# Performance work log

Hardware: AMD Instinct MI355X
Metric: run time of the kernel (lower is better)

Reference implementation:

```python
import jax, jax.numpy as jnp
import numpy as np

B, N, DIM, HEADS = 2, 2048, 1024, 16
HD = DIM // HEADS
STEPS, DT = 10, 0.1
PI = np.float32(np.pi)
SCALE = HD ** -0.5


def l2norm(x, eps=1e-12):
    # torch F.normalize: x / max(||x||_2, eps), works for complex via |x|^2
    n = jnp.sqrt(jnp.sum(jnp.abs(x) ** 2, axis=-1, keepdims=True))
    return x / jnp.maximum(n, eps)


def setup_inputs() -> dict:
    key = jax.random.key(0)
    ks = jax.random.split(key, 6)
    x = jax.random.normal(ks[0], (B, N, DIM), dtype=jnp.float32)
    Wqkv = jax.random.normal(ks[1], (DIM, 3 * DIM), dtype=jnp.float32) * (DIM ** -0.5)
    bqkv = jnp.zeros((3 * DIM,), dtype=jnp.float32)
    Wp1 = jax.random.normal(ks[2], (HD, 2 * HD), dtype=jnp.float32) * (HD ** -0.5)
    bp1 = jnp.zeros((2 * HD,), dtype=jnp.float32)
    Wp2 = jax.random.normal(ks[3], (2 * HD, HD), dtype=jnp.float32) * ((2 * HD) ** -0.5)
    bp2 = jnp.zeros((HD,), dtype=jnp.float32)
    Wf = jax.random.normal(ks[4], (HD, HD), dtype=jnp.float32) * (HD ** -0.5)
    return {"x": x, "Wqkv": Wqkv, "bqkv": bqkv, "Wp1": Wp1, "bp1": bp1,
            "Wp2": Wp2, "bp2": bp2, "Wf": Wf}


def _forward(x, Wqkv, bqkv, Wp1, bp1, Wp2, bp2, Wf):
    # qkv projection + normalize over last dim of the concatenated qkv
    qkv = l2norm(x @ Wqkv + bqkv)                      # [B,N,3*DIM]
    q, k, v = jnp.split(qkv, 3, axis=-1)

    def split_heads(t):
        return t.reshape(B, N, HEADS, HD).transpose(0, 2, 1, 3)  # [B,H,N,D]

    q, k, v = split_heads(q), split_heads(k), split_heads(v)

    def prepare_quantum_state(t):
        phase = jnp.tanh(t @ Wp1 + bp1) @ Wp2 + bp2    # phase-net MLP
        amplitude = l2norm(t)
        phase = jnp.tanh(phase) * PI
        return amplitude * jnp.exp(1j * phase)         # complex64 state

    q, k, v = prepare_quantum_state(q), prepare_quantum_state(k), prepare_quantum_state(v)

    def geometric_flow(z):
        # 10-step Euler integration of linear geometric velocity field
        for _ in range(STEPS):
            z = z + DT * (z @ Wf.astype(z.dtype))
        return l2norm(z)

    q = geometric_flow(q)
    k = geometric_flow(k)

    # parallel_transport(k, q): complex elementwise square -> complex dist
    diff = k - q
    dist = jnp.sqrt(jnp.sum(diff * diff, axis=-1, keepdims=True))
    tf = 1.0 / (1.0 + jnp.exp(10.0 * dist))            # sigmoid(-10*dist)
    k_t = l2norm(k * tf + q * (1.0 - tf))

    dots = (jnp.einsum('bhnd,bhmd->bhnm', q, k_t) * SCALE).real
    attn = jax.nn.softmax(dots, axis=-1)               # dropout in eval mode
    v = jnp.abs(v)                                     # magnitude of values
    out = jnp.einsum('bhnm,bhmd->bhnd', attn, v)
    return out.transpose(0, 2, 1, 3).reshape(B, N, DIM)


def reference(x, Wqkv, bqkv, Wp1, bp1, Wp2, bp2, Wf):
    return _forward(x, Wqkv, bqkv, Wp1, bp1, Wp2, bp2, Wf)
```

## Files before the change

kernel.cpp:

```cpp
#include <hip/hip_runtime.h>
#include <math.h>

#define B_    2
#define N_    2048
#define DIM_  1024
#define H_    16
#define HD_   64
#define TDIM  3072
#define ROWS  4096
#define PI_F  3.14159265358979323846f
#define SCALE_F 0.125f

typedef short short8 __attribute__((ext_vector_type(8)));
typedef float f32x4 __attribute__((ext_vector_type(4)));
typedef float f32x16 __attribute__((ext_vector_type(16)));
typedef unsigned u32x4 __attribute__((ext_vector_type(4)));
typedef unsigned short ushort_t;

__device__ __forceinline__ float wave_sum(float v) {
#pragma unroll
  for (int off = 32; off > 0; off >>= 1) v += __shfl_xor(v, off, 64);
  return v;
}

__device__ __forceinline__ unsigned short f2bf(float x) {
  return (unsigned short)((__float_as_uint(x) + 0x8000u) >> 16);
}
__device__ __forceinline__ float bf2f(unsigned short h) {
  return __uint_as_float(((unsigned)h) << 16);
}
__device__ __forceinline__ float inv_norm(float s) {
  return __builtin_amdgcn_rsqf(fmaxf(s, 1e-24f));
}
__device__ __forceinline__ float fast_tanh(float x) {
  return 1.0f - 2.0f / (__expf(2.0f * x) + 1.0f);
}

__device__ __forceinline__ void gl_lds16(const void* g, void* l) {
  __builtin_amdgcn_global_load_lds(
      (const __attribute__((address_space(1))) unsigned int*)g,
      (__attribute__((address_space(3))) unsigned int*)l, 16, 0, 0);
}

__global__ __launch_bounds__(256) void zero_sumsq(float* __restrict__ s) {
  const int i = threadIdx.x;
#pragma unroll
  for (int j = 0; j < 16; ++j) s[j * 256 + i] = 0.0f;
}

__global__ __launch_bounds__(256) void compute_M(const float* __restrict__ Wf,
                                                 ushort_t* __restrict__ Ms) {
  __shared__ float P[4096], Q[4096], R[4096];
  const int tid = threadIdx.x;
  for (int i = tid; i < 4096; i += 256)
    P[i] = 0.1f * Wf[i] + (((i >> 6) == (i & 63)) ? 1.0f : 0.0f);
  __syncthreads();

#define MATMUL64(X, Y, Z) \
  for (int i = tid; i < 4096; i += 256) { \
    const int r_ = i >> 6, c_ = i & 63; \
    float s0 = 0.f, s1 = 0.f, s2 = 0.f, s3 = 0.f; \
    _Pragma("unroll") \
    for (int e = 0; e < 64; e += 4) { \
      s0 = fmaf(X[r_ * 64 + e],     Y[e * 64 + c_], s0); \
      s1 = fmaf(X[r_ * 64 + e + 1], Y[(e + 1) * 64 + c_], s1); \
      s2 = fmaf(X[r_ * 64 + e + 2], Y[(e + 2) * 64 + c_], s2); \
      s3 = fmaf(X[r_ * 64 + e + 3], Y[(e + 3) * 64 + c_], s3); \
    } \
    Z[i] = (s0 + s1) + (s2 + s3); \
  } \
  __syncthreads();

  MATMUL64(P, P, Q)
  MATMUL64(Q, Q, R)
  MATMUL64(R, R, P)
  MATMUL64(P, Q, R)
#undef MATMUL64

  for (int i = tid; i < 4096; i += 256) {
    const int n = i >> 6, k = i & 63;
    const float v = R[k * 64 + n];
    const ushort_t hi = f2bf(v);
    Ms[i] = hi; Ms[4096 + i] = f2bf(v - bf2f(hi));
  }
}

__global__ __launch_bounds__(256) void prep_w(const float* __restrict__ Wp1,
                                              const float* __restrict__ Wp2,
                                              ushort_t* __restrict__ W1s,
                                              ushort_t* __restrict__ W2s) {
  const int tid = threadIdx.x;
  for (int i = tid; i < 8192; i += 256) {
    const int n = i >> 6, k = i & 63;
    const float v = Wp1[k * 128 + n];
    const ushort_t hi = f2bf(v);
    W1s[i] = hi; W1s[8192 + i] = f2bf(v - bf2f(hi));
  }
  for (int i = tid; i < 8192; i += 256) {
    const int n = i >> 7, k = i & 127;
    const float v = Wp2[k * 64 + n];
    const ushort_t hi = f2bf(v);
    W2s[i] = hi; W2s[8192 + i] = f2bf(v - bf2f(hi));
  }
}

__global__ __launch_bounds__(256) void split_X(const float* __restrict__ X,
                                               unsigned short* __restrict__ Xs) {
  const int gid = blockIdx.x * 256 + threadIdx.x;
  const int m = gid >> 8, c = (gid & 255) * 4;
  float4 v = *(const float4*)&X[(size_t)m * 1024 + c];
  ushort4 hi, lo;
  hi.x = f2bf(v.x); lo.x = f2bf(v.x - bf2f(hi.x));
  hi.y = f2bf(v.y); lo.y = f2bf(v.y - bf2f(hi.y));
  hi.z = f2bf(v.z); lo.z = f2bf(v.z - bf2f(hi.z));
  hi.w = f2bf(v.w); lo.w = f2bf(v.w - bf2f(hi.w));
  *(ushort4*)&Xs[(size_t)m * 2048 + c] = hi;
  *(ushort4*)&Xs[(size_t)m * 2048 + 1024 + c] = lo;
}

__global__ __launch_bounds__(256) void split_W(const float* __restrict__ W,
                                               unsigned short* __restrict__ Wt) {
  __shared__ float T[64][68];
  const int n0 = blockIdx.x * 64, k0 = blockIdx.y * 64;
  const int tid = threadIdx.x;
  for (int l = tid; l < 1024; l += 256) {
    const int r = l >> 4, c = (l & 15) * 4;
    *(float4*)&T[r][c] = *(const float4*)&W[(size_t)(k0 + r) * TDIM + n0 + c];
  }
  __syncthreads();
  const int n = tid >> 2, q = (tid & 3) * 16;
  alignas(16) unsigned short hi16[16];
  alignas(16) unsigned short lo16[16];
#pragma unroll
  for (int j = 0; j < 16; ++j) {
    const float v = T[q + j][n];
    const unsigned short h = f2bf(v);
    hi16[j] = h; lo16[j] = f2bf(v - bf2f(h));
  }
  unsigned short* dst = &Wt[(size_t)(n0 + n) * 2048];
  *(uint4*)&dst[k0 + q]          = *(uint4*)&hi16[0];
  *(uint4*)&dst[k0 + q + 8]      = *(uint4*)&hi16[8];
  *(uint4*)&dst[1024 + k0 + q]     = *(uint4*)&lo16[0];
  *(uint4*)&dst[1024 + k0 + q + 8] = *(uint4*)&lo16[8];
}

__global__ __launch_bounds__(512, 2) void gemm8(const unsigned short* __restrict__ Xs,
                                                const unsigned short* __restrict__ Wt,
                                                const float* __restrict__ bias,
                                                float* __restrict__ C,
                                                float* __restrict__ sumsq) {
  __shared__ __align__(16) ushort_t Ab[2][256 * 64];
  __shared__ __align__(16) ushort_t Bb[2][256 * 64];
  const int tid = threadIdx.x;
  const int wv = tid >> 6, ln = tid & 63;
  const int l16 = ln & 15, quad = ln >> 4;
  const int wm = wv >> 2, wn = wv & 3;
  const int row0 = blockIdx.y * 256, col0 = blockIdx.x * 256;
  const int lr = ln >> 3, sg8 = (ln & 7) ^ lr;

  f32x4 acc[8][4];
#pragma unroll
  for (int i = 0; i < 8; ++i)
#pragma unroll
    for (int j = 0; j < 4; ++j) acc[i][j] = {0.f, 0.f, 0.f, 0.f};

#define STAGE_SG(sg, tt, AB, BB) do { \
    const int t_ = (tt); \
    const int k_ = t_ / 3, p_ = t_ - k_ * 3; \
    const int ka_ = (p_ == 2 ? 1024 : 0) + k_ * 64; \
    const int kb_ = (p_ == 1 ? 1024 : 0) + k_ * 64; \
    if ((sg) == 0 || (sg) == 3) { \
      _Pragma("unroll") for (int j_ = 0; j_ < 2; ++j_) { \
        const int r0_ = ((sg) == 0 ? (j_ ? 128 : 0) : (j_ ? 192 : 64)) + wv * 8; \
        gl_lds16(&Xs[(size_t)(row0 + r0_ + lr) * 2048 + ka_ + sg8 * 8], \
                 (char*)((AB) + r0_ * 64)); \
      } \
    } else { \
      _Pragma("unroll") for (int j_ = 0; j_ < 2; ++j_) { \
        const int m_ = j_ * 8 + wv; \
        const int r0_ = (m_ >> 2) * 64 + (m_ & 3) * 8 + ((sg) == 2 ? 32 : 0); \
        gl_lds16(&Wt[(size_t)(col0 + r0_ + lr) * 2048 + kb_ + sg8 * 8], \
                 (char*)((BB) + r0_ * 64)); \
      } \
    } \
  } while (0)

#define LDA(mh) do { \
    _Pragma("unroll") for (int mi_ = 0; mi_ < 4; ++mi_) { \
      const int rr_ = wm * 128 + (mh) * 64 + mi_ * 16 + l16; \
      _Pragma("unroll") for (int kk_ = 0; kk_ < 2; ++kk_) \
        afr[mi_][kk_] = *(const short8*)&As[rr_ * 64 + (((kk_ * 4 + quad) ^ (l16 & 7)) * 8)]; \
    } \
  } while (0)

#define LDB(nh) do { \
    _Pragma("unroll") for (int j_ = 0; j_ < 2; ++j_) { \
      const int rr_ = wn * 64 + ((nh) * 2 + j_) * 16 + l16; \
      _Pragma("unroll") for (int kk_ = 0; kk_ < 2; ++kk_) \
        bfr[(nh) * 2 + j_][kk_] = *(const short8*)&Bs[rr_ * 64 + (((kk_ * 4 + quad) ^ (l16 & 7)) * 8)]; \
    } \
  } while (0)

#define MFMA_Q(mh, nh) do { \
    _Pragma("unroll") for (int mi_ = 0; mi_ < 4; ++mi_) \
    _Pragma("unroll") for (int j_ = 0; j_ < 2; ++j_) \
    _Pragma("unroll") for (int kk_ = 0; kk_ < 2; ++kk_) \
      acc[(mh) * 4 + mi_][(nh) * 2 + j_] = __builtin_amdgcn_mfma_f32_16x16x32_bf16( \
          afr[mi_][kk_], bfr[(nh) * 2 + j_][kk_], acc[(mh) * 4 + mi_][(nh) * 2 + j_], 0, 0, 0); \
  } while (0)

  STAGE_SG(0, 0, Ab[0], Bb[0]);
  STAGE_SG(1, 0, Ab[0], Bb[0]);
  STAGE_SG(2, 0, Ab[0], Bb[0]);
  STAGE_SG(3, 0, Ab[0], Bb[0]);
  STAGE_SG(0, 1, Ab[1], Bb[1]);
  STAGE_SG(1, 1, Ab[1], Bb[1]);
  STAGE_SG(2, 1, Ab[1], Bb[1]);
  asm volatile("s_waitcnt vmcnt(6)");
  __builtin_amdgcn_s_barrier();

  short8 afr[4][2], bfr[4][2];
  for (int t = 0; t < 48; ++t) {
    ushort_t* As = Ab[t & 1];
    ushort_t* Bs = Bb[t & 1];
    ushort_t* An = Ab[(t + 1) & 1];
    ushort_t* Bn = Bb[(t + 1) & 1];

    LDA(0);
    LDB(0);
    if (t + 1 < 48) STAGE_SG(3, t + 1, An, Bn);
    __builtin_amdgcn_s_barrier();
    asm volatile("s_waitcnt lgkmcnt(0)");
    __builtin_amdgcn_sched_barrier(0);
    __builtin_amdgcn_s_setprio(1);
    MFMA_Q(0, 0);
    __builtin_amdgcn_s_setprio(0);
    __builtin_amdgcn_s_barrier();

    LDB(1);
    if (t + 2 < 48) STAGE_SG(0, t + 2, As, Bs);
    __builtin_amdgcn_s_barrier();
    asm volatile("s_waitcnt lgkmcnt(0)");
    __builtin_amdgcn_sched_barrier(0);
    __builtin_amdgcn_s_setprio(1);
    MFMA_Q(0, 1);
    __builtin_amdgcn_s_setprio(0);
    __builtin_amdgcn_s_barrier();

    LDA(1);
    if (t + 2 < 48) STAGE_SG(1, t + 2, As, Bs);
    __builtin_amdgcn_s_barrier();
    asm volatile("s_waitcnt lgkmcnt(0)");
    __builtin_amdgcn_sched_barrier(0);
    __builtin_amdgcn_s_setprio(1);
    MFMA_Q(1, 0);
    __builtin_amdgcn_s_setprio(0);
    __builtin_amdgcn_s_barrier();

    if (t + 2 < 48) STAGE_SG(2, t + 2, As, Bs);
    __builtin_amdgcn_s_barrier();
    __builtin_amdgcn_s_setprio(1);
    MFMA_Q(1, 1);
    __builtin_amdgcn_s_setprio(0);
    if (t < 46) asm volatile("s_waitcnt vmcnt(6)");
    else        asm volatile("s_waitcnt vmcnt(0)");
    __builtin_amdgcn_sched_barrier(0);
    __builtin_amdgcn_s_barrier();
  }
#undef STAGE_SG
#undef LDA
#undef LDB
#undef MFMA_Q

  float ps[8][4];
#pragma unroll
  for (int m8 = 0; m8 < 8; ++m8)
#pragma unroll
    for (int r = 0; r < 4; ++r) ps[m8][r] = 0.f;
#pragma unroll
  for (int ni = 0; ni < 4; ++ni) {
    const int col = col0 + wn * 64 + ni * 16 + l16;
    const float bb = bias[col];
#pragma unroll
    for (int m8 = 0; m8 < 8; ++m8) {
#pragma unroll
      for (int r = 0; r < 4; ++r) {
        const int row = row0 + wm * 128 + m8 * 16 + quad * 4 + r;
        const float o = acc[m8][ni][r] + bb;
        C[(size_t)row * TDIM + col] = o;
        ps[m8][r] = fmaf(o, o, ps[m8][r]);
      }
    }
  }
#pragma unroll
  for (int m8 = 0; m8 < 8; ++m8) {
#pragma unroll
    for (int r = 0; r < 4; ++r) {
      float v = ps[m8][r];
      v += __shfl_xor(v, 1, 64);
      v += __shfl_xor(v, 2, 64);
      v += __shfl_xor(v, 4, 64);
      v += __shfl_xor(v, 8, 64);
      if (l16 == 0)
        atomicAdd(&sumsq[row0 + wm * 128 + m8 * 16 + quad * 4 + r], v);
    }
  }
}

__global__ __launch_bounds__(256, 4) void prep_wave(
    const float* __restrict__ qkv, const float* __restrict__ sumsq,
    const ushort_t* __restrict__ W1s, const float* __restrict__ bp1,
    const ushort_t* __restrict__ W2s, const float* __restrict__ bp2,
    const ushort_t* __restrict__ Ms,
    ushort_t* __restrict__ Qc, ushort_t* __restrict__ Kc,
    ushort_t* __restrict__ Vt) {
  __shared__ __align__(16) char smem[4 * 6912];
  const int tid = threadIdx.x;
  const int wv = tid >> 6, ln = tid & 63;
  const int l16 = ln & 15, quad = ln >> 4;
  char* wscr = smem + wv * 6912;
  ushort_t (*T)[72]   = (ushort_t(*)[72])(wscr);
  ushort_t (*Hs)[136] = (ushort_t(*)[136])(wscr + 2304);
  ushort_t (*Vs)[72]  = (ushort_t(*)[72])(wscr + 2304);
  ushort_t (*Z)[16][72] = (ushort_t(*)[16][72])(wscr + 2304);

  const int gw = blockIdx.x * 4 + wv;
  const int p0 = gw * 8;
  const int bh = p0 >> 11, n0 = p0 & 2047;
  const int b = bh >> 4, h = bh & 15;

  short8 aTh[2], aTl[2];
  float invt_l;
  {
    const int tp = l16 & 7, tisk = l16 >> 3;
    const size_t tb = ((size_t)(b * N_ + n0 + tp)) * TDIM + h * HD_ +
                      tisk * 1024 + quad * 8;
    const float inv = inv_norm(sumsq[b * N_ + n0 + tp]);
    float tvv[16];
    float4 t0 = *(const float4*)&qkv[tb];
    float4 t1 = *(const float4*)&qkv[tb + 4];
    float4 t2 = *(const float4*)&qkv[tb + 32];
    float4 t3 = *(const float4*)&qkv[tb + 36];
    tvv[0]=t0.x*inv; tvv[1]=t0.y*inv; tvv[2]=t0.z*inv; tvv[3]=t0.w*inv;
    tvv[4]=t1.x*inv; tvv[5]=t1.y*inv; tvv[6]=t1.z*inv; tvv[7]=t1.w*inv;
    tvv[8]=t2.x*inv; tvv[9]=t2.y*inv; tvv[10]=t2.z*inv; tvv[11]=t2.w*inv;
    tvv[12]=t3.x*inv; tvv[13]=t3.y*inv; tvv[14]=t3.z*inv; tvv[15]=t3.w*inv;
    float s = 0.f;
#pragma unroll
    for (int j = 0; j < 16; ++j) s = fmaf(tvv[j], tvv[j], s);
    s += __shfl_xor(s, 16, 64);
    s += __shfl_xor(s, 32, 64);
    invt_l = inv_norm(s);
    alignas(16) ushort_t hh[16];
    alignas(16) ushort_t llo[16];
#pragma unroll
    for (int j = 0; j < 16; ++j) {
      hh[j] = f2bf(tvv[j]);
      llo[j] = f2bf(tvv[j] - bf2f(hh[j]));
    }
    aTh[0] = *(const short8*)&hh[0]; aTh[1] = *(const short8*)&hh[8];
    aTl[0] = *(const short8*)&llo[0]; aTl[1] = *(const short8*)&llo[8];
    *(uint4*)&T[l16][quad * 8]      = *(const uint4*)&hh[0];
    *(uint4*)&T[l16][32 + quad * 8] = *(const uint4*)&hh[8];
  }
  {
    const int vp = ln >> 3, vc = (ln & 7) * 8;
    const size_t vb = ((size_t)(b * N_ + n0 + vp)) * TDIM + h * HD_ + 2048 + vc;
    float vv[8];
    float4 v0 = *(const float4*)&qkv[vb];
    float4 v1 = *(const float4*)&qkv[vb + 4];
    vv[0]=v0.x; vv[1]=v0.y; vv[2]=v0.z; vv[3]=v0.w;
    vv[4]=v1.x; vv[5]=v1.y; vv[6]=v1.z; vv[7]=v1.w;
    float sv = 0.f;
#pragma unroll
    for (int j = 0; j < 8; ++j) sv = fmaf(vv[j], vv[j], sv);
    sv += __shfl_xor(sv, 1, 64);
    sv += __shfl_xor(sv, 2, 64);
    sv += __shfl_xor(sv, 4, 64);
    const float vinv = inv_norm(sv);
    alignas(16) ushort_t vb16[8];
#pragma unroll
    for (int j = 0; j < 8; ++j) vb16[j] = f2bf(fabsf(vv[j]) * vinv);
    *(uint4*)&Vs[vp][vc] = *(const uint4*)&vb16[0];
    alignas(16) ushort_t ov[8];
#pragma unroll
    for (int p = 0; p < 8; ++p) ov[p] = Vs[p][ln];
    *(uint4*)&Vt[((size_t)(bh * 64) + ln) * N_ + n0] = *(const uint4*)&ov[0];
  }
  float invt_r[4];
#pragma unroll
  for (int r = 0; r < 4; ++r) invt_r[r] = __shfl(invt_l, quad * 4 + r, 64);

#pragma unroll
  for (int ct = 0; ct < 8; ++ct) {
    const int colg = ct * 16 + l16;
    f32x4 c = {0.f, 0.f, 0.f, 0.f};
#pragma unroll
    for (int s = 0; s < 2; ++s) {
      short8 wh = *(const short8*)&W1s[(size_t)colg * 64 + s * 32 + quad * 8];
      short8 wl = *(const short8*)&W1s[8192 + (size_t)colg * 64 + s * 32 + quad * 8];
      c = __builtin_amdgcn_mfma_f32_16x16x32_bf16(aTh[s], wh, c, 0, 0, 0);
      c = __builtin_amdgcn_mfma_f32_16x16x32_bf16(aTh[s], wl, c, 0, 0, 0);
      c = __builtin_amdgcn_mfma_f32_16x16x32_bf16(aTl[s], wh, c, 0, 0, 0);
    }
    const float bb = bp1[colg];
#pragma unroll
    for (int r = 0; r < 4; ++r)
      Hs[quad * 4 + r][colg] = f2bf(fast_tanh(c[r] + bb));
  }

  {
    short8 aH[4];
#pragma unroll
    for (int s = 0; s < 4; ++s)
      aH[s] = *(const short8*)&Hs[l16][s * 32 + quad * 8];
#pragma unroll
    for (int ct = 0; ct < 4; ++ct) {
      const int d = ct * 16 + l16;
      f32x4 c = {0.f, 0.f, 0.f, 0.f};
#pragma unroll
      for (int s = 0; s < 4; ++s) {
        short8 wh = *(const short8*)&W2s[(size_t)d * 128 + s * 32 + quad * 8];
        short8 wl = *(const short8*)&W2s[8192 + (size_t)d * 128 + s * 32 + quad * 8];
        c = __builtin_amdgcn_mfma_f32_16x16x32_bf16(aH[s], wh, c, 0, 0, 0);
        c = __builtin_amdgcn_mfma_f32_16x16x32_bf16(aH[s], wl, c, 0, 0, 0);
      }
      const float b2v = bp2[d];
#pragma unroll
      for (int r = 0; r < 4; ++r) {
        const int row = quad * 4 + r;
        const float ph = fast_tanh(c[r] + b2v) * PI_F;
        const float amp = bf2f(T[row][d]) * invt_r[r];
        float sp, cp;
        __sincosf(ph, &sp, &cp);
        Z[0][row][d] = f2bf(amp * cp);
        Z[1][row][d] = f2bf(amp * sp);
      }
    }
  }

  f32x4 cc[2][4];
  {
    short8 aZ[2][2];
#pragma unroll
    for (int comp = 0; comp < 2; ++comp)
#pragma unroll
      for (int s = 0; s < 2; ++s)
        aZ[comp][s] = *(const short8*)&Z[comp][l16][s * 32 + quad * 8];
#pragma unroll
    for (int ct = 0; ct < 4; ++ct) {
      const int colg = ct * 16 + l16;
      short8 mh[2], ml[2];
#pragma unroll
      for (int s = 0; s < 2; ++s) {
        mh[s] = *(const short8*)&Ms[(size_t)colg * 64 + s * 32 + quad * 8];
        ml[s] = *(const short8*)&Ms[4096 + (size_t)colg * 64 + s * 32 + quad * 8];
      }
#pragma unroll
      for (int comp = 0; comp < 2; ++comp) {
        f32x4 c = {0.f, 0.f, 0.f, 0.f};
#pragma unroll
        for (int s = 0; s < 2; ++s) {
          c = __builtin_amdgcn_mfma_f32_16x16x32_bf16(aZ[comp][s], mh[s], c, 0, 0, 0);
          c = __builtin_amdgcn_mfma_f32_16x16x32_bf16(aZ[comp][s], ml[s], c, 0, 0, 0);
        }
        cc[comp][ct] = c;
      }
    }
  }

  const bool isk = quad >= 2;
#pragma unroll
  for (int r = 0; r < 4; ++r) {
    float fr[4], fi[4];
#pragma unroll
    for (int ct = 0; ct < 4; ++ct) { fr[ct] = cc[0][ct][r]; fi[ct] = cc[1][ct][r]; }
    float s = 0.f;
#pragma unroll
    for (int ct = 0; ct < 4; ++ct) s += fmaf(fr[ct], fr[ct], fi[ct] * fi[ct]);
    s += __shfl_xor(s, 1, 64); s += __shfl_xor(s, 2, 64);
    s += __shfl_xor(s, 4, 64); s += __shfl_xor(s, 8, 64);
    const float invn_ = inv_norm(s);
#pragma unroll
    for (int ct = 0; ct < 4; ++ct) { fr[ct] *= invn_; fi[ct] *= invn_; }
    float or_[4], oi_[4];
#pragma unroll
    for (int ct = 0; ct < 4; ++ct) {
      or_[ct] = __shfl_xor(fr[ct], 32, 64);
      oi_[ct] = __shfl_xor(fi[ct], 32, 64);
    }
    float qr[4], qi[4], kr[4], ki[4];
#pragma unroll
    for (int ct = 0; ct < 4; ++ct) {
      qr[ct] = isk ? or_[ct] : fr[ct];
      qi[ct] = isk ? oi_[ct] : fi[ct];
      kr[ct] = isk ? fr[ct] : or_[ct];
      ki[ct] = isk ? fi[ct] : oi_[ct];
    }
    float sA = 0.f, sB = 0.f;
    float dr[4], di[4];
#pragma unroll
    for (int ct = 0; ct < 4; ++ct) {
      dr[ct] = kr[ct] - qr[ct];
      di[ct] = ki[ct] - qi[ct];
      sA += fmaf(dr[ct], dr[ct], -di[ct] * di[ct]);
      sB += 2.0f * dr[ct] * di[ct];
    }
    sA += __shfl_xor(sA, 1, 64); sA += __shfl_xor(sA, 2, 64);
    sA += __shfl_xor(sA, 4, 64); sA += __shfl_xor(sA, 8, 64);
    sB += __shfl_xor(sB, 1, 64); sB += __shfl_xor(sB, 2, 64);
    sB += __shfl_xor(sB, 4, 64); sB += __shfl_xor(sB, 8, 64);
    const float rad = sqrtf(fmaf(sA, sA, sB * sB));
    const float ur = sqrtf(fmaxf((rad + sA) * 0.5f, 0.0f));
    const float ui = copysignf(sqrtf(fmaxf((rad - sA) * 0.5f, 0.0f)), sB);
    const float er = __expf(10.0f * ur);
    float s10, c10;
    __sincosf(10.0f * ui, &s10, &c10);
    const float exr = er * c10, exi = er * s10;
    const float dnr = 1.0f + exr, dni = exi;
    const float rd2 = __builtin_amdgcn_rcpf(fmaf(dnr, dnr, dni * dni));
    const float tfr = dnr * rd2, tfi = -dni * rd2;
    const float omr = 1.0f - tfr, omi = -tfi;
    float ktr[4], kti[4];
    float s2 = 0.f;
#pragma unroll
    for (int ct = 0; ct < 4; ++ct) {
      ktr[ct] = kr[ct] * tfr - ki[ct] * tfi + qr[ct] * omr - qi[ct] * omi;
      kti[ct] = kr[ct] * tfi + ki[ct] * tfr + qr[ct] * omi + qi[ct] * omr;
      s2 += fmaf(ktr[ct], ktr[ct], kti[ct] * kti[ct]);
    }
    s2 += __shfl_xor(s2, 1, 64); s2 += __shfl_xor(s2, 2, 64);
    s2 += __shfl_xor(s2, 4, 64); s2 += __shfl_xor(s2, 8, 64);
    const float inv2 = inv_norm(s2);
    const int p = (quad & 1) * 4 + r;
    const size_t o = ((size_t)bh * N_ + n0 + p) * 128;
    if (!isk) {
#pragma unroll
      for (int ct = 0; ct < 4; ++ct) {
        const int d = ct * 16 + l16;
        Qc[o + d]      = f2bf(qr[ct]);
        Qc[o + 64 + d] = f2bf(qi[ct]);
      }
    } else {
#pragma unroll
      for (int ct = 0; ct < 4; ++ct) {
        const int d = ct * 16 + l16;
        Kc[o + d]      = f2bf(ktr[ct] * inv2);
        Kc[o + 64 + d] = f2bf(-kti[ct] * inv2);
      }
    }
  }
}

__global__ __launch_bounds__(256, 2) void attn3(
    const ushort_t* __restrict__ Qc, const ushort_t* __restrict__ Kc,
    const ushort_t* __restrict__ Vt, float* __restrict__ out) {
  __shared__ __align__(16) char smem[35328];
  ushort_t* Ks = (ushort_t*)smem;
  ushort_t* Vs = (ushort_t*)(smem + 16384);
  float (*Of)[68] = (float(*)[68])smem;
  float* Dd = (float*)(smem + 34816);

  const int tid = threadIdx.x;
  const int wv = tid >> 6, ln = tid & 63;
  const int l31 = ln & 31, hi = ln >> 5;
  const int qh = wv & 1, kh = wv >> 1;
  const int bh = blockIdx.y;
  const int q0 = blockIdx.x * 128;
  const size_t hb = (size_t)bh * N_;

  short8 qf[2][8];
#pragma unroll
  for (int nt = 0; nt < 2; ++nt) {
    const size_t qrow = (hb + q0 + qh * 64 + nt * 32 + l31) * 128;
#pragma unroll
    for (int s = 0; s < 8; ++s)
      qf[nt][s] = *(const short8*)&Qc[qrow + s * 16 + hi * 8];
  }

  f32x16 oacc[2][2];
#pragma unroll
  for (int i = 0; i < 2; ++i)
#pragma unroll
    for (int j = 0; j < 2; ++j)
#pragma unroll
      for (int r = 0; r < 16; ++r) oacc[i][j][r] = 0.f;
  float den[2] = {0.f, 0.f};

  const int rK = kh * 32 + l31;
  for (int kt = 0; kt < N_ / 64; ++kt) {
    const size_t kbase = (hb + kt * 64) * 128;
    __syncthreads();
#pragma unroll
    for (int i = 0; i < 4; ++i) {
      const int l = tid + i * 256;
      const int r = l >> 4, c = l & 15;
      uint4 v = *(const uint4*)&Kc[kbase + (size_t)r * 128 + c * 8];
      *(uint4*)&Ks[r * 128 + ((c ^ (r & 15)) * 8)] = v;
    }
#pragma unroll
    for (int i = 0; i < 2; ++i) {
      const int l = tid + i * 256;
      const int r = l >> 3, c = l & 7;
      uint4 v = *(const uint4*)&Vt[((size_t)bh * 64 + r) * N_ + kt * 64 + c * 8];
      *(uint4*)&Vs[r * 128 + ((c ^ (r & 15)) * 8)] = v;
    }
    __syncthreads();

    f32x16 sacc[2];
#pragma unroll
    for (int nt = 0; nt < 2; ++nt)
#pragma unroll
      for (int r = 0; r < 16; ++r) sacc[nt][r] = 0.f;
#pragma unroll
    for (int s = 0; s < 8; ++s) {
      const int c = s * 2 + hi;
      short8 ak = *(const short8*)&Ks[rK * 128 + ((c ^ (rK & 15)) * 8)];
      sacc[0] = __builtin_amdgcn_mfma_f32_32x32x16_bf16(ak, qf[0][s], sacc[0], 0, 0, 0);
      sacc[1] = __builtin_amdgcn_mfma_f32_32x32x16_bf16(ak, qf[1][s], sacc[1], 0, 0, 0);
    }

    short8 pfrag[2][2];
#pragma unroll
    for (int nt = 0; nt < 2; ++nt) {
      float pv[16];
      float dl = 0.f;
#pragma unroll
      for (int r = 0; r < 16; ++r) {
        pv[r] = __expf(sacc[nt][r] * SCALE_F);
        dl += pv[r];
      }
      den[nt] += dl;
      unsigned u8a[8], pu[8];
#pragma unroll
      for (int t = 0; t < 8; ++t)
        u8a[t] = (unsigned)f2bf(pv[2 * t]) | ((unsigned)f2bf(pv[2 * t + 1]) << 16);
#pragma unroll
      for (int t = 0; t < 8; ++t)
        pu[t] = (unsigned)__shfl_xor((int)u8a[t], 32, 64);
#pragma unroll
      for (int s2 = 0; s2 < 2; ++s2) {
        u32x4 fu;
        if (hi == 0) {
          fu[0] = u8a[4 * s2]; fu[1] = u8a[4 * s2 + 1];
          fu[2] = pu[4 * s2];  fu[3] = pu[4 * s2 + 1];
        } else {
          fu[0] = pu[4 * s2 + 2];  fu[1] = pu[4 * s2 + 3];
          fu[2] = u8a[4 * s2 + 2]; fu[3] = u8a[4 * s2 + 3];
        }
        pfrag[nt][s2] = __builtin_bit_cast(short8, fu);
      }
    }

#pragma unroll
    for (int s2 = 0; s2 < 2; ++s2) {
#pragma unroll
      for (int dt = 0; dt < 2; ++dt) {
        const int rV = dt * 32 + l31;
        const int c = kh * 4 + s2 * 2 + hi;
        short8 bv = *(const short8*)&Vs[rV * 128 + ((c ^ (rV & 15)) * 8)];
        oacc[0][dt] = __builtin_amdgcn_mfma_f32_32x32x16_bf16(pfrag[0][s2], bv, oacc[0][dt], 0, 0, 0);
        oacc[1][dt] = __builtin_amdgcn_mfma_f32_32x32x16_bf16(pfrag[1][s2], bv, oacc[1][dt], 0, 0, 0);
      }
    }
  }

#pragma unroll
  for (int nt = 0; nt < 2; ++nt)
    den[nt] += __shfl_xor(den[nt], 32, 64);

  __syncthreads();
  if (kh == 0) {
#pragma unroll
    for (int nt = 0; nt < 2; ++nt) {
#pragma unroll
      for (int dt = 0; dt < 2; ++dt)
#pragma unroll
        for (int r = 0; r < 16; ++r) {
          const int row = qh * 64 + nt * 32 + (r & 3) + 8 * (r >> 2) + 4 * hi;
          Of[row][dt * 32 + l31] = oacc[nt][dt][r];
        }
      if (hi == 0) Dd[qh * 64 + nt * 32 + l31] = den[nt];
    }
  }
  __syncthreads();
  if (kh == 1) {
#pragma unroll
    for (int nt = 0; nt < 2; ++nt) {
#pragma unroll
      for (int dt = 0; dt < 2; ++dt)
#pragma unroll
        for (int r = 0; r < 16; ++r) {
          const int row = qh * 64 + nt * 32 + (r & 3) + 8 * (r >> 2) + 4 * hi;
          Of[row][dt * 32 + l31] += oacc[nt][dt][r];
        }
      if (hi == 0) Dd[qh * 64 + nt * 32 + l31] += den[nt];
    }
  }
  __syncthreads();

  {
    const int ql = tid >> 1, half = tid & 1;
    const int b = bh >> 4, h = bh & 15;
    const float invd = __builtin_amdgcn_rcpf(Dd[ql]);
    float* op = &out[(((size_t)b * N_ + q0 + ql) * H_ + h) * HD_ + half * 32];
#pragma unroll
    for (int j = 0; j < 8; ++j) {
      float4 o = *(const float4*)&Of[ql][half * 32 + j * 4];
      o.x *= invd; o.y *= invd; o.z *= invd; o.w *= invd;
      *(float4*)&op[j * 4] = o;
    }
  }
}

extern "C" void kernel_launch(void* const* d_in, const int* in_sizes, int n_in,
                              void* d_out, int out_size, void* d_ws, size_t ws_size,
                              hipStream_t stream) {
  const float* x    = (const float*)d_in[0];
  const float* Wqkv = (const float*)d_in[1];
  const float* bqkv = (const float*)d_in[2];
  const float* Wp1  = (const float*)d_in[3];
  const float* bp1  = (const float*)d_in[4];
  const float* Wp2  = (const float*)d_in[5];
  const float* bp2  = (const float*)d_in[6];
  const float* Wf   = (const float*)d_in[7];
  float* out = (float*)d_out;

  char* w = (char*)d_ws;
  float* qkv = (float*)w;               w += (size_t)ROWS * TDIM * 4;
  float* sumsq = (float*)w;             w += (size_t)ROWS * 4;
  ushort_t* Ms  = (ushort_t*)w;         w += 2 * 4096 * 2;
  ushort_t* W1s = (ushort_t*)w;         w += 2 * 8192 * 2;
  ushort_t* W2s = (ushort_t*)w;         w += 2 * 8192 * 2;
  unsigned short* Xs = (unsigned short*)w; w += (size_t)ROWS * 2048 * 2;
  unsigned short* Wt = (unsigned short*)w; w += (size_t)TDIM * 2048 * 2;
  unsigned short* Qc = (unsigned short*)w; w += (size_t)32 * N_ * 128 * 2;
  unsigned short* Kc = (unsigned short*)w; w += (size_t)32 * N_ * 128 * 2;
  unsigned short* Vt = (unsigned short*)w; w += (size_t)32 * 64 * N_ * 2;

  hipLaunchKernelGGL(split_X, dim3(ROWS * 1024 / 4 / 256), dim3(256), 0, stream, x, Xs);
  hipLaunchKernelGGL(split_W, dim3(48, 16), dim3(256), 0, stream, Wqkv, Wt);
  hipLaunchKernelGGL(compute_M, dim3(1), dim3(256), 0, stream, Wf, Ms);
  hipLaunchKernelGGL(prep_w, dim3(1), dim3(256), 0, stream, Wp1, Wp2, W1s, W2s);
  hipLaunchKernelGGL(zero_sumsq, dim3(1), dim3(256), 0, stream, sumsq);
  hipLaunchKernelGGL(gemm8, dim3(12, 16), dim3(512), 0, stream, Xs, Wt, bqkv, qkv, sumsq);
  hipLaunchKernelGGL(prep_wave, dim3(2048), dim3(256), 0, stream,
                     qkv, sumsq, W1s, bp1, W2s, bp2, Ms, Qc, Kc, Vt);
  hipLaunchKernelGGL(attn3, dim3(N_ / 128, B_ * H_), dim3(256), 0, stream,
                     Qc, Kc, Vt, out);
}
```

Measured before the change: 387.2 us.

## Retile QKV GEMM to 256x192 blocks with shared A-hi reuse and swizzled grid

Measured after the change: 366.0 us. -5.5%, faster.

```diff
diff --git a/kernel.cpp b/kernel.cpp
--- a/kernel.cpp
+++ b/kernel.cpp
@@ -48,17 +48,19 @@
   for (int j = 0; j < 16; ++j) s[j * 256 + i] = 0.0f;
 }
 
-__global__ __launch_bounds__(256) void compute_M(const float* __restrict__ Wf,
-                                                 ushort_t* __restrict__ Ms) {
+__global__ __launch_bounds__(1024) void compute_M(const float* __restrict__ Wf,
+                                                  ushort_t* __restrict__ Ms) {
   __shared__ float P[4096], Q[4096], R[4096];
   const int tid = threadIdx.x;
-  for (int i = tid; i < 4096; i += 256)
+  for (int i = tid; i < 4096; i += 1024)
     P[i] = 0.1f * Wf[i] + (((i >> 6) == (i & 63)) ? 1.0f : 0.0f);
   __syncthreads();
 
 #define MATMUL64(X, Y, Z) \
-  for (int i = tid; i < 4096; i += 256) { \
-    const int r_ = i >> 6, c_ = i & 63; \
+  _Pragma("unroll") \
+  for (int jo = 0; jo < 4; ++jo) { \
+    const int i_ = tid + jo * 1024; \
+    const int r_ = i_ >> 6, c_ = i_ & 63; \
     float s0 = 0.f, s1 = 0.f, s2 = 0.f, s3 = 0.f; \
     _Pragma("unroll") \
     for (int e = 0; e < 64; e += 4) { \
@@ -67,7 +69,7 @@
       s2 = fmaf(X[r_ * 64 + e + 2], Y[(e + 2) * 64 + c_], s2); \
       s3 = fmaf(X[r_ * 64 + e + 3], Y[(e + 3) * 64 + c_], s3); \
     } \
-    Z[i] = (s0 + s1) + (s2 + s3); \
+    Z[i_] = (s0 + s1) + (s2 + s3); \
   } \
   __syncthreads();
 
@@ -77,7 +79,7 @@
   MATMUL64(P, Q, R)
 #undef MATMUL64
 
-  for (int i = tid; i < 4096; i += 256) {
+  for (int i = tid; i < 4096; i += 1024) {
     const int n = i >> 6, k = i & 63;
     const float v = R[k * 64 + n];
     const ushort_t hi = f2bf(v);
@@ -144,165 +146,162 @@
   *(uint4*)&dst[1024 + k0 + q + 8] = *(uint4*)&lo16[8];
 }
 
-__global__ __launch_bounds__(512, 2) void gemm8(const unsigned short* __restrict__ Xs,
+#define BAR   __builtin_amdgcn_s_barrier()
+#define LGKM  asm volatile("s_waitcnt lgkmcnt(0)")
+#define SB    __builtin_amdgcn_sched_barrier(0)
+#define PRIO1 __builtin_amdgcn_s_setprio(1)
+#define PRIO0 __builtin_amdgcn_s_setprio(0)
+#define WAITV(n) asm volatile("s_waitcnt vmcnt(" #n ")")
+
+__global__ __launch_bounds__(512, 2) void gemm9(const unsigned short* __restrict__ Xs,
                                                 const unsigned short* __restrict__ Wt,
                                                 const float* __restrict__ bias,
                                                 float* __restrict__ C,
                                                 float* __restrict__ sumsq) {
   __shared__ __align__(16) ushort_t Ab[2][256 * 64];
-  __shared__ __align__(16) ushort_t Bb[2][256 * 64];
+  __shared__ __align__(16) ushort_t Bb0[192 * 64];
+  __shared__ __align__(16) ushort_t Bb1[192 * 64];
   const int tid = threadIdx.x;
   const int wv = tid >> 6, ln = tid & 63;
   const int l16 = ln & 15, quad = ln >> 4;
-  const int wm = wv >> 2, wn = wv & 3;
-  const int row0 = blockIdx.y * 256, col0 = blockIdx.x * 256;
+  const int wm = wv >> 1, wn = wv & 1;
+  const int flat = blockIdx.x;
+  const int swz = (flat & 7) * 32 + (flat >> 3);
+  const int row0 = (swz >> 4) * 256, col0 = (swz & 15) * 192;
   const int lr = ln >> 3, sg8 = (ln & 7) ^ lr;
 
-  f32x4 acc[8][4];
-#pragma unroll
-  for (int i = 0; i < 8; ++i)
-#pragma unroll
-    for (int j = 0; j < 4; ++j) acc[i][j] = {0.f, 0.f, 0.f, 0.f};
-
-#define STAGE_SG(sg, tt, AB, BB) do { \
-    const int t_ = (tt); \
-    const int k_ = t_ / 3, p_ = t_ - k_ * 3; \
-    const int ka_ = (p_ == 2 ? 1024 : 0) + k_ * 64; \
-    const int kb_ = (p_ == 1 ? 1024 : 0) + k_ * 64; \
-    if ((sg) == 0 || (sg) == 3) { \
-      _Pragma("unroll") for (int j_ = 0; j_ < 2; ++j_) { \
-        const int r0_ = ((sg) == 0 ? (j_ ? 128 : 0) : (j_ ? 192 : 64)) + wv * 8; \
-        gl_lds16(&Xs[(size_t)(row0 + r0_ + lr) * 2048 + ka_ + sg8 * 8], \
-                 (char*)((AB) + r0_ * 64)); \
-      } \
-    } else { \
-      _Pragma("unroll") for (int j_ = 0; j_ < 2; ++j_) { \
-        const int m_ = j_ * 8 + wv; \
-        const int r0_ = (m_ >> 2) * 64 + (m_ & 3) * 8 + ((sg) == 2 ? 32 : 0); \
-        gl_lds16(&Wt[(size_t)(col0 + r0_ + lr) * 2048 + kb_ + sg8 * 8], \
-                 (char*)((BB) + r0_ * 64)); \
-      } \
+  f32x4 acc[4][6];
+#pragma unroll
+  for (int i = 0; i < 4; ++i)
+#pragma unroll
+    for (int j = 0; j < 6; ++j) acc[i][j] = {0.f, 0.f, 0.f, 0.f};
+
+#define STAGE_A(dstBuf, koff) do { \
+    _Pragma("unroll") for (int j_ = 0; j_ < 4; ++j_) { \
+      const int g_ = wv + j_ * 8; \
+      gl_lds16(&Xs[(size_t)(row0 + g_ * 8 + lr) * 2048 + (koff) + sg8 * 8], \
+               (char*)(dstBuf) + g_ * 1024); \
     } \
   } while (0)
-
-#define LDA(mh) do { \
-    _Pragma("unroll") for (int mi_ = 0; mi_ < 4; ++mi_) { \
-      const int rr_ = wm * 128 + (mh) * 64 + mi_ * 16 + l16; \
-      _Pragma("unroll") for (int kk_ = 0; kk_ < 2; ++kk_) \
-        afr[mi_][kk_] = *(const short8*)&As[rr_ * 64 + (((kk_ * 4 + quad) ^ (l16 & 7)) * 8)]; \
+#define STAGE_B(dstBuf, koff) do { \
+    _Pragma("unroll") for (int j_ = 0; j_ < 3; ++j_) { \
+      const int g_ = wv + j_ * 8; \
+      gl_lds16(&Wt[(size_t)(col0 + g_ * 8 + lr) * 2048 + (koff) + sg8 * 8], \
+               (char*)(dstBuf) + g_ * 1024); \
     } \
   } while (0)
 
-#define LDB(nh) do { \
+#define LDA(Abuf, mh) do { \
     _Pragma("unroll") for (int j_ = 0; j_ < 2; ++j_) { \
-      const int rr_ = wn * 64 + ((nh) * 2 + j_) * 16 + l16; \
+      const int rr_ = wm * 64 + (mh) * 32 + j_ * 16 + l16; \
       _Pragma("unroll") for (int kk_ = 0; kk_ < 2; ++kk_) \
-        bfr[(nh) * 2 + j_][kk_] = *(const short8*)&Bs[rr_ * 64 + (((kk_ * 4 + quad) ^ (l16 & 7)) * 8)]; \
+        afr[j_][kk_] = *(const short8*)&(Abuf)[rr_ * 64 + (((kk_ * 4 + quad) ^ (l16 & 7)) * 8)]; \
     } \
   } while (0)
 
+#define LDB(Bbuf, nh) do { \
+    _Pragma("unroll") for (int j_ = 0; j_ < 3; ++j_) { \
+      const int rr_ = wn * 96 + (nh) * 48 + j_ * 16 + l16; \
+      _Pragma("unroll") for (int kk_ = 0; kk_ < 2; ++kk_) \
+        bfr[(nh) * 3 + j_][kk_] = *(const short8*)&(Bbuf)[rr_ * 64 + (((kk_ * 4 + quad) ^ (l16 & 7)) * 8)]; \
+    } \
+  } while (0)
+
 #define MFMA_Q(mh, nh) do { \
-    _Pragma("unroll") for (int mi_ = 0; mi_ < 4; ++mi_) \
     _Pragma("unroll") for (int j_ = 0; j_ < 2; ++j_) \
+    _Pragma("unroll") for (int i_ = 0; i_ < 3; ++i_) \
     _Pragma("unroll") for (int kk_ = 0; kk_ < 2; ++kk_) \
-      acc[(mh) * 4 + mi_][(nh) * 2 + j_] = __builtin_amdgcn_mfma_f32_16x16x32_bf16( \
-          afr[mi_][kk_], bfr[(nh) * 2 + j_][kk_], acc[(mh) * 4 + mi_][(nh) * 2 + j_], 0, 0, 0); \
+      acc[(mh) * 2 + j_][(nh) * 3 + i_] = __builtin_amdgcn_mfma_f32_16x16x32_bf16( \
+          afr[j_][kk_], bfr[(nh) * 3 + i_][kk_], acc[(mh) * 2 + j_][(nh) * 3 + i_], 0, 0, 0); \
   } while (0)
 
-  STAGE_SG(0, 0, Ab[0], Bb[0]);
-  STAGE_SG(1, 0, Ab[0], Bb[0]);
-  STAGE_SG(2, 0, Ab[0], Bb[0]);
-  STAGE_SG(3, 0, Ab[0], Bb[0]);
-  STAGE_SG(0, 1, Ab[1], Bb[1]);
-  STAGE_SG(1, 1, Ab[1], Bb[1]);
-  STAGE_SG(2, 1, Ab[1], Bb[1]);
-  asm volatile("s_waitcnt vmcnt(6)");
-  __builtin_amdgcn_s_barrier();
-
-  short8 afr[4][2], bfr[4][2];
-  for (int t = 0; t < 48; ++t) {
-    ushort_t* As = Ab[t & 1];
-    ushort_t* Bs = Bb[t & 1];
-    ushort_t* An = Ab[(t + 1) & 1];
-    ushort_t* Bn = Bb[(t + 1) & 1];
-
-    LDA(0);
-    LDB(0);
-    if (t + 1 < 48) STAGE_SG(3, t + 1, An, Bn);
-    __builtin_amdgcn_s_barrier();
-    asm volatile("s_waitcnt lgkmcnt(0)");
-    __builtin_amdgcn_sched_barrier(0);
-    __builtin_amdgcn_s_setprio(1);
-    MFMA_Q(0, 0);
-    __builtin_amdgcn_s_setprio(0);
-    __builtin_amdgcn_s_barrier();
-
-    LDB(1);
-    if (t + 2 < 48) STAGE_SG(0, t + 2, As, Bs);
-    __builtin_amdgcn_s_barrier();
-    asm volatile("s_waitcnt lgkmcnt(0)");
-    __builtin_amdgcn_sched_barrier(0);
-    __builtin_amdgcn_s_setprio(1);
-    MFMA_Q(0, 1);
-    __builtin_amdgcn_s_setprio(0);
-    __builtin_amdgcn_s_barrier();
-
-    LDA(1);
-    if (t + 2 < 48) STAGE_SG(1, t + 2, As, Bs);
-    __builtin_amdgcn_s_barrier();
-    asm volatile("s_waitcnt lgkmcnt(0)");
-    __builtin_amdgcn_sched_barrier(0);
-    __builtin_amdgcn_s_setprio(1);
-    MFMA_Q(1, 0);
-    __builtin_amdgcn_s_setprio(0);
-    __builtin_amdgcn_s_barrier();
-
-    if (t + 2 < 48) STAGE_SG(2, t + 2, As, Bs);
-    __builtin_amdgcn_s_barrier();
-    __builtin_amdgcn_s_setprio(1);
-    MFMA_Q(1, 1);
-    __builtin_amdgcn_s_setprio(0);
-    if (t < 46) asm volatile("s_waitcnt vmcnt(6)");
-    else        asm volatile("s_waitcnt vmcnt(0)");
-    __builtin_amdgcn_sched_barrier(0);
-    __builtin_amdgcn_s_barrier();
-  }
-#undef STAGE_SG
+  STAGE_B(Bb0, 0);
+  STAGE_A(Ab[0], 0);
+  STAGE_A(Ab[1], 1024);
+  STAGE_B(Bb1, 1024);
+  WAITV(7);
+  BAR;
+
+  short8 afr[2][2], bfr[6][2];
+#pragma unroll 2
+  for (int k = 0; k < 16; ++k) {
+    ushort_t* Ahi = Ab[k & 1];
+    ushort_t* Alo = Ab[(k & 1) ^ 1];
+    const int kn = (k + 1) * 64;
+    const bool more = (k < 15);
+
+    LDA(Ahi, 0); LDB(Bb0, 0);
+    BAR; LGKM; SB; PRIO1; MFMA_Q(0, 0); PRIO0; BAR;
+    LDB(Bb0, 1);
+    BAR; LGKM; SB; PRIO1; MFMA_Q(0, 1); PRIO0; BAR;
+    LDA(Ahi, 1);
+    BAR; LGKM; SB; PRIO1; MFMA_Q(1, 0); PRIO0; BAR;
+    PRIO1; MFMA_Q(1, 1); PRIO0;
+    WAITV(3);
+    SB; BAR;
+
+    LDA(Alo, 0); LDB(Bb0, 0);
+    BAR; LGKM; SB; PRIO1; MFMA_Q(0, 0); PRIO0; BAR;
+    LDB(Bb0, 1);
+    BAR; LGKM; SB; PRIO1; MFMA_Q(0, 1); PRIO0; BAR;
+    LDA(Alo, 1);
+    if (more) STAGE_B(Bb0, kn);
+    BAR; LGKM; SB; PRIO1; MFMA_Q(1, 0); PRIO0; BAR;
+    if (more) STAGE_A(Alo, kn);
+    SB; PRIO1; MFMA_Q(1, 1); PRIO0;
+    if (more) { WAITV(7); }
+    else      { WAITV(0); }
+    SB; BAR;
+
+    LDA(Ahi, 0); LDB(Bb1, 0);
+    BAR; LGKM; SB; PRIO1; MFMA_Q(0, 0); PRIO0; BAR;
+    LDB(Bb1, 1);
+    BAR; LGKM; SB; PRIO1; MFMA_Q(0, 1); PRIO0; BAR;
+    LDA(Ahi, 1);
+    BAR; LGKM; SB; PRIO1; MFMA_Q(1, 0); PRIO0; BAR;
+    if (more) { STAGE_A(Ahi, 1024 + kn); STAGE_B(Bb1, 1024 + kn); }
+    SB; PRIO1; MFMA_Q(1, 1); PRIO0;
+    if (more) { WAITV(7); }
+    else      { WAITV(0); }
+    SB; BAR;
+  }
+#undef STAGE_A
+#undef STAGE_B
 #undef LDA
 #undef LDB
 #undef MFMA_Q
 
-  float ps[8][4];
-#pragma unroll
-  for (int m8 = 0; m8 < 8; ++m8)
-#pragma unroll
-    for (int r = 0; r < 4; ++r) ps[m8][r] = 0.f;
-#pragma unroll
-  for (int ni = 0; ni < 4; ++ni) {
-    const int col = col0 + wn * 64 + ni * 16 + l16;
+  float ps[4][4];
+#pragma unroll
+  for (int mi = 0; mi < 4; ++mi)
+#pragma unroll
+    for (int r = 0; r < 4; ++r) ps[mi][r] = 0.f;
+#pragma unroll
+  for (int ni = 0; ni < 6; ++ni) {
+    const int col = col0 + wn * 96 + ni * 16 + l16;
     const float bb = bias[col];
 #pragma unroll
-    for (int m8 = 0; m8 < 8; ++m8) {
+    for (int mi = 0; mi < 4; ++mi) {
 #pragma unroll
       for (int r = 0; r < 4; ++r) {
-        const int row = row0 + wm * 128 + m8 * 16 + quad * 4 + r;
-        const float o = acc[m8][ni][r] + bb;
+        const int row = row0 + wm * 64 + mi * 16 + quad * 4 + r;
+        const float o = acc[mi][ni][r] + bb;
         C[(size_t)row * TDIM + col] = o;
-        ps[m8][r] = fmaf(o, o, ps[m8][r]);
-      }
-    }
-  }
-#pragma unroll
-  for (int m8 = 0; m8 < 8; ++m8) {
+        ps[mi][r] = fmaf(o, o, ps[mi][r]);
+      }
+    }
+  }
+#pragma unroll
+  for (int mi = 0; mi < 4; ++mi) {
 #pragma unroll
     for (int r = 0; r < 4; ++r) {
-      float v = ps[m8][r];
+      float v = ps[mi][r];
       v += __shfl_xor(v, 1, 64);
       v += __shfl_xor(v, 2, 64);
       v += __shfl_xor(v, 4, 64);
       v += __shfl_xor(v, 8, 64);
       if (l16 == 0)
-        atomicAdd(&sumsq[row0 + wm * 128 + m8 * 16 + quad * 4 + r], v);
+        atomicAdd(&sumsq[row0 + wm * 64 + mi * 16 + quad * 4 + r], v);
     }
   }
 }
@@ -740,10 +739,10 @@
 
   hipLaunchKernelGGL(split_X, dim3(ROWS * 1024 / 4 / 256), dim3(256), 0, stream, x, Xs);
   hipLaunchKernelGGL(split_W, dim3(48, 16), dim3(256), 0, stream, Wqkv, Wt);
-  hipLaunchKernelGGL(compute_M, dim3(1), dim3(256), 0, stream, Wf, Ms);
+  hipLaunchKernelGGL(compute_M, dim3(1), dim3(1024), 0, stream, Wf, Ms);
   hipLaunchKernelGGL(prep_w, dim3(1), dim3(256), 0, stream, Wp1, Wp2, W1s, W2s);
   hipLaunchKernelGGL(zero_sumsq, dim3(1), dim3(256), 0, stream, sumsq);
-  hipLaunchKernelGGL(gemm8, dim3(12, 16), dim3(512), 0, stream, Xs, Wt, bqkv, qkv, sumsq);
+  hipLaunchKernelGGL(gemm9, dim3(256), dim3(512), 0, stream, Xs, Wt, bqkv, qkv, sumsq);
   hipLaunchKernelGGL(prep_wave, dim3(2048), dim3(256), 0, stream,
                      qkv, sumsq, W1s, bp1, W2s, bp2, Ms, Qc, Kc, Vt);
   hipLaunchKernelGGL(attn3, dim3(N_ / 128, B_ * H_), dim3(256), 0, stream,
```
